# Kernel optimization log

Measured on AMD Instinct MI355X. Metric: run time of the kernel, lower is better.

Reference implementation:

```python
import jax, jax.numpy as jnp
import numpy as np

N = 33554432  # 32M elements, 128 MB fp32

def setup_inputs() -> dict:
    key = jax.random.key(0)
    inp = jax.random.uniform(key, (N,), dtype=jnp.float32)
    return {"inp": inp}

def reference(inp) -> jnp.ndarray:
    # Faithful to the original: exp(x) / sum(exp(inp)) with NO max-subtraction
    # (the torch module computes the unstabilized softmax).
    e = jnp.exp(inp)
    return e / jnp.sum(e)
```

## Files before the change

kernel.cpp:

```cpp
#include <hip/hip_runtime.h>


#define BLOCK 256
#define RGRID 2048
#define SGRID 2048

typedef float vfloat4 __attribute__((ext_vector_type(4)));

__global__ __launch_bounds__(BLOCK) void softmax_reduce(
    const float* __restrict__ inp, float* __restrict__ partials, int n4) {
  const vfloat4* __restrict__ in4 = (const vfloat4*)inp;
  int tid = blockIdx.x * BLOCK + threadIdx.x;
  int stride = gridDim.x * BLOCK;

  float s0 = 0.0f, s1 = 0.0f;
  int i = tid;
  for (; i + stride < n4; i += 2 * stride) {
    vfloat4 a = in4[i];
    vfloat4 b = in4[i + stride];
    s0 += __expf(a.x) + __expf(a.y) + __expf(a.z) + __expf(a.w);
    s1 += __expf(b.x) + __expf(b.y) + __expf(b.z) + __expf(b.w);
  }
  for (; i < n4; i += stride) {
    vfloat4 a = in4[i];
    s0 += __expf(a.x) + __expf(a.y) + __expf(a.z) + __expf(a.w);
  }
  float s = s0 + s1;

  #pragma unroll
  for (int off = 32; off > 0; off >>= 1)
    s += __shfl_down(s, off, 64);

  __shared__ float wsum[BLOCK / 64];
  if ((threadIdx.x & 63) == 0) wsum[threadIdx.x >> 6] = s;
  __syncthreads();
  if (threadIdx.x == 0)
    partials[blockIdx.x] = wsum[0] + wsum[1] + wsum[2] + wsum[3];
}

__global__ __launch_bounds__(BLOCK) void softmax_scale(
    const float* __restrict__ inp, float* __restrict__ out,
    const float* __restrict__ partials, int n4) {
  float t = 0.0f;
  #pragma unroll
  for (int i = 0; i < RGRID / BLOCK; ++i)
    t += partials[i * BLOCK + threadIdx.x];

  #pragma unroll
  for (int off = 32; off > 0; off >>= 1)
    t += __shfl_down(t, off, 64);

  __shared__ float wsum[BLOCK / 64];
  if ((threadIdx.x & 63) == 0) wsum[threadIdx.x >> 6] = t;
  __syncthreads();
  float r = 1.0f / (wsum[0] + wsum[1] + wsum[2] + wsum[3]);

  const vfloat4* __restrict__ in4 = (const vfloat4*)inp;
  vfloat4* __restrict__ out4 = (vfloat4*)out;
  int tid = blockIdx.x * BLOCK + threadIdx.x;
  int stride = gridDim.x * BLOCK;

  int i = tid;
  for (; i + stride < n4; i += 2 * stride) {
    vfloat4 a = in4[i];
    vfloat4 b = in4[i + stride];
    vfloat4 oa, ob;
    oa.x = __expf(a.x) * r; oa.y = __expf(a.y) * r;
    oa.z = __expf(a.z) * r; oa.w = __expf(a.w) * r;
    ob.x = __expf(b.x) * r; ob.y = __expf(b.y) * r;
    ob.z = __expf(b.z) * r; ob.w = __expf(b.w) * r;
    __builtin_nontemporal_store(oa, &out4[i]);
    __builtin_nontemporal_store(ob, &out4[i + stride]);
  }
  for (; i < n4; i += stride) {
    vfloat4 a = in4[i];
    vfloat4 oa;
    oa.x = __expf(a.x) * r; oa.y = __expf(a.y) * r;
    oa.z = __expf(a.z) * r; oa.w = __expf(a.w) * r;
    __builtin_nontemporal_store(oa, &out4[i]);
  }
}

extern "C" void kernel_launch(void* const* d_in, const int* in_sizes, int n_in,
                              void* d_out, int out_size, void* d_ws, size_t ws_size,
                              hipStream_t stream) {
  const float* inp = (const float*)d_in[0];
  float* out = (float*)d_out;
  float* partials = (float*)d_ws;
  int n = in_sizes[0];
  int n4 = n >> 2;

  softmax_reduce<<<RGRID, BLOCK, 0, stream>>>(inp, partials, n4);
  softmax_scale<<<SGRID, BLOCK, 0, stream>>>(inp, out, partials, n4);
}
```

Measured before the change: 247.6 us.

## Fuse reduce and scale into one cooperative kernel with grid sync

Merges the two-pass softmax into one cooperative kernel: each block sums exp over its slice, writes a partial, waits at a grid-wide sync, then reduces all partials and writes the scaled output. This drops the second kernel launch and the gap between launches, and the grid shrinks to 1024 blocks to fit the co-residency limit. The 128 MB input is still read twice, since it cannot stay in cache. The grid barrier and the smaller grid may cost throughput, and if a cooperative launch of 1024 blocks is rejected the kernel does not run.

```diff
diff --git a/kernel.cpp b/kernel.cpp
--- a/kernel.cpp
+++ b/kernel.cpp
@@ -1,17 +1,23 @@
 #include <hip/hip_runtime.h>
+#include <hip/hip_cooperative_groups.h>
 
 
 #define BLOCK 256
-#define RGRID 2048
-#define SGRID 2048
+#define GRID 1024
 
 typedef float vfloat4 __attribute__((ext_vector_type(4)));
 
-__global__ __launch_bounds__(BLOCK) void softmax_reduce(
-    const float* __restrict__ inp, float* __restrict__ partials, int n4) {
+namespace cg = cooperative_groups;
+
+__global__ __launch_bounds__(BLOCK) void softmax_fused(
+    const float* __restrict__ inp, float* __restrict__ out,
+    float* __restrict__ partials, int n4) {
   const vfloat4* __restrict__ in4 = (const vfloat4*)inp;
+  vfloat4* __restrict__ out4 = (vfloat4*)out;
   int tid = blockIdx.x * BLOCK + threadIdx.x;
-  int stride = gridDim.x * BLOCK;
+  int stride = GRID * BLOCK;
+
+  __shared__ float wsum[BLOCK / 64];
 
   float s0 = 0.0f, s1 = 0.0f;
   int i = tid;
@@ -31,36 +37,27 @@
   for (int off = 32; off > 0; off >>= 1)
     s += __shfl_down(s, off, 64);
 
-  __shared__ float wsum[BLOCK / 64];
   if ((threadIdx.x & 63) == 0) wsum[threadIdx.x >> 6] = s;
   __syncthreads();
   if (threadIdx.x == 0)
     partials[blockIdx.x] = wsum[0] + wsum[1] + wsum[2] + wsum[3];
-}
 
-__global__ __launch_bounds__(BLOCK) void softmax_scale(
-    const float* __restrict__ inp, float* __restrict__ out,
-    const float* __restrict__ partials, int n4) {
+  cg::this_grid().sync();
+
   float t = 0.0f;
   #pragma unroll
-  for (int i = 0; i < RGRID / BLOCK; ++i)
-    t += partials[i * BLOCK + threadIdx.x];
+  for (int k = 0; k < GRID / BLOCK; ++k)
+    t += partials[k * BLOCK + threadIdx.x];
 
   #pragma unroll
   for (int off = 32; off > 0; off >>= 1)
     t += __shfl_down(t, off, 64);
 
-  __shared__ float wsum[BLOCK / 64];
   if ((threadIdx.x & 63) == 0) wsum[threadIdx.x >> 6] = t;
   __syncthreads();
   float r = 1.0f / (wsum[0] + wsum[1] + wsum[2] + wsum[3]);
 
-  const vfloat4* __restrict__ in4 = (const vfloat4*)inp;
-  vfloat4* __restrict__ out4 = (vfloat4*)out;
-  int tid = blockIdx.x * BLOCK + threadIdx.x;
-  int stride = gridDim.x * BLOCK;
-
-  int i = tid;
+  i = tid;
   for (; i + stride < n4; i += 2 * stride) {
     vfloat4 a = in4[i];
     vfloat4 b = in4[i + stride];
@@ -90,6 +87,7 @@
   int n = in_sizes[0];
   int n4 = n >> 2;
 
-  softmax_reduce<<<RGRID, BLOCK, 0, stream>>>(inp, partials, n4);
-  softmax_scale<<<SGRID, BLOCK, 0, stream>>>(inp, out, partials, n4);
+  void* args[] = {(void*)&inp, (void*)&out, (void*)&partials, (void*)&n4};
+  hipLaunchCooperativeKernel((void*)softmax_fused, dim3(GRID), dim3(BLOCK),
+                             args, 0, stream);
 }
```

Measured after the change: 340.5 us. +37.5%, slower.
